# Optimization experiments

Hardware: AMD Instinct MI355X
Metric: run time of the kernel (lower is better)

The kernel has to match this reference:

```python
import jax, jax.numpy as jnp
import numpy as np

NUM_EVT = 8192
NUM_SEVT = 16384
EMBED_DIM = 128


def setup_inputs() -> dict:
    key = jax.random.key(0)
    k_adj, k_sub, k_evt, k_w = jax.random.split(key, 4)
    adj = jax.random.uniform(k_adj, (NUM_EVT, NUM_SEVT), dtype=jnp.float32)
    subevent = jax.random.normal(k_sub, (NUM_SEVT, EMBED_DIM), dtype=jnp.float32)
    event = jax.random.normal(k_evt, (NUM_EVT, EMBED_DIM), dtype=jnp.float32)
    # attn_fc: Linear(2*D -> 1, bias=False), xavier_uniform; stored flat as [2*D]
    bound = float(np.sqrt(6.0 / (2 * EMBED_DIM + 1)))
    attn_w = jax.random.uniform(k_w, (2 * EMBED_DIM,), dtype=jnp.float32,
                                minval=-bound, maxval=bound)
    return {"adj": adj, "subevent": subevent, "event": event, "attn_w": attn_w}


def reference(adj, subevent, event, attn_w):
    D = subevent.shape[-1]
    # concat order in torch forward: [sevt, evt] -> first D weights hit subevent
    a_s, a_e = attn_w[:D], attn_w[D:]
    s_proj = subevent @ a_s            # [S]
    e_proj = event @ a_e               # [E]
    # score(e,s) = LeakyReLU( attn_fc([adj*sub_s ; adj*evt_e]) )
    #            = LeakyReLU( adj[e,s] * (e_proj[e] + s_proj[s]) )
    scores = jax.nn.leaky_relu(adj * (e_proj[:, None] + s_proj[None, :]), 0.2)  # [E,S]
    attn = jax.nn.softmax(scores, axis=-1)                                      # [E,S]
    # sum_s attn[e,s] * (adj[e,s] * subevent[s])
    sevt_evt = (attn * adj) @ subevent                                          # [E,D]
    out = (event + sevt_evt) * 0.5
    return out.astype(subevent.dtype)
```

## Files before the change

### kernel.cpp

```cpp
#include <hip/hip_runtime.h>

typedef __attribute__((ext_vector_type(4))) float float4v;
typedef __attribute__((ext_vector_type(8))) short short8;

#define NEVT 8192
#define NSEVT 16384
#define DIM 128
#define BM 16
#define BK 128
#define NTILE (NSEVT / BK)

__device__ __forceinline__ unsigned f2bf(float f) {
  unsigned u = __builtin_bit_cast(unsigned, f);
  return (u + 0x7FFFu + ((u >> 16) & 1u)) >> 16;
}

__global__ void proj_kernel(const float* __restrict__ event,
                            const float* __restrict__ subevent,
                            const float* __restrict__ attn_w,
                            float* __restrict__ eproj,
                            float* __restrict__ sproj) {
  int gw = (int)((blockIdx.x * blockDim.x + threadIdx.x) >> 6);
  int lane = threadIdx.x & 63;
  const float* row;
  const float* w;
  float* outp;
  if (gw < NEVT) {
    row = event + (size_t)gw * DIM;
    w = attn_w + DIM;
    outp = eproj + gw;
  } else {
    row = subevent + (size_t)(gw - NEVT) * DIM;
    w = attn_w;
    outp = sproj + (gw - NEVT);
  }
  float2 x = *(const float2*)(row + lane * 2);
  float2 ww = *(const float2*)(w + lane * 2);
  float p = x.x * ww.x + x.y * ww.y;
#pragma unroll
  for (int off = 32; off > 0; off >>= 1) p += __shfl_down(p, off, 64);
  if (lane == 0) *outp = p;
}

__global__ void frag_kernel(const float* __restrict__ sub,
                            unsigned short* __restrict__ frag) {
  int tid = blockIdx.x * 256 + threadIdx.x;
  int lane = tid & 63;
  int db = (tid >> 6) & 7;
  int kt = tid >> 9;
  int r0 = kt * 32 + ((lane >> 4) << 3);
  int col = db * 16 + (lane & 15);
  unsigned pk[4];
#pragma unroll
  for (int jj = 0; jj < 4; ++jj) {
    unsigned lo = f2bf(sub[(size_t)(r0 + 2 * jj) * DIM + col]);
    unsigned hi = f2bf(sub[(size_t)(r0 + 2 * jj + 1) * DIM + col]);
    pk[jj] = lo | (hi << 16);
  }
  uint4 v = {pk[0], pk[1], pk[2], pk[3]};
  *(uint4*)(frag + (size_t)tid * 8) = v;
}

__global__ __launch_bounds__(256, 2) void fused_kernel(
    const float* __restrict__ adj, const float* __restrict__ event,
    const unsigned short* __restrict__ subfrag, const float* __restrict__ eproj,
    const float* __restrict__ sproj, float* __restrict__ out) {
  __shared__ unsigned short P[2][BM][132];
  __shared__ float dsum[BM][32];

  const int t = threadIdx.x;
  const int lane = t & 63;
  const int wave = t >> 6;
  const int r0 = blockIdx.x * BM;
  const int rA = t >> 5;
  const int cL = (t & 31) * 4;
  const int m = lane & 15;
  const int q = lane >> 4;

  const float ep0 = eproj[r0 + rA];
  const float ep1 = eproj[r0 + rA + 8];

  const float* adj0 = adj + (size_t)(r0 + rA) * NSEVT + cL;
  const float* adj1 = adj + (size_t)(r0 + rA + 8) * NSEVT + cL;

  float4v a0 = *(const float4v*)(adj0);
  float4v a1 = *(const float4v*)(adj1);
  float4v sp = *(const float4v*)(sproj + cL);

  float4v acc0 = {0.f, 0.f, 0.f, 0.f};
  float4v acc1 = {0.f, 0.f, 0.f, 0.f};
  float d0 = 0.f, d1 = 0.f;

  for (int tile = 0; tile < NTILE; ++tile) {
    short8 bf[4][2];
#pragma unroll
    for (int ks = 0; ks < 4; ++ks) {
#pragma unroll
      for (int i = 0; i < 2; ++i) {
        size_t off =
            ((size_t)((tile * 4 + ks) * 8 + (wave * 2 + i)) * 64 + lane) * 8;
        bf[ks][i] = *(const short8*)(subfrag + off);
      }
    }
    float4v na0 = a0, na1 = a1, nsp = sp;
    if (tile + 1 < NTILE) {
      na0 = *(const float4v*)(adj0 + (size_t)(tile + 1) * BK);
      na1 = *(const float4v*)(adj1 + (size_t)(tile + 1) * BK);
      nsp = *(const float4v*)(sproj + (tile + 1) * BK + cL);
    }
    unsigned pkA0, pkA1, pkB0, pkB1;
    {
      float w[4];
#pragma unroll
      for (int c = 0; c < 4; ++c) {
        float x = a0[c] * (ep0 + sp[c]);
        float y = fmaxf(x, 0.2f * x);
        float p = __builtin_amdgcn_exp2f(y * 1.442695040888963f);
        d0 += p;
        w[c] = p * a0[c];
      }
      pkA0 = f2bf(w[0]) | (f2bf(w[1]) << 16);
      pkA1 = f2bf(w[2]) | (f2bf(w[3]) << 16);
#pragma unroll
      for (int c = 0; c < 4; ++c) {
        float x = a1[c] * (ep1 + sp[c]);
        float y = fmaxf(x, 0.2f * x);
        float p = __builtin_amdgcn_exp2f(y * 1.442695040888963f);
        d1 += p;
        w[c] = p * a1[c];
      }
      pkB0 = f2bf(w[0]) | (f2bf(w[1]) << 16);
      pkB1 = f2bf(w[2]) | (f2bf(w[3]) << 16);
    }
    const int buf = tile & 1;
    uint2 v0 = {pkA0, pkA1};
    *(uint2*)&P[buf][rA][cL] = v0;
    uint2 v1 = {pkB0, pkB1};
    *(uint2*)&P[buf][rA + 8][cL] = v1;

    __syncthreads();

#pragma unroll
    for (int ks = 0; ks < 4; ++ks) {
      const unsigned short* ap = &P[buf][m][q * 8 + ks * 32];
      uint2 lo = *(const uint2*)(ap);
      uint2 hi = *(const uint2*)(ap + 4);
      uint4 au = {lo.x, lo.y, hi.x, hi.y};
      short8 af = __builtin_bit_cast(short8, au);
      acc0 = __builtin_amdgcn_mfma_f32_16x16x32_bf16(af, bf[ks][0], acc0, 0, 0, 0);
      acc1 = __builtin_amdgcn_mfma_f32_16x16x32_bf16(af, bf[ks][1], acc1, 0, 0, 0);
    }
    a0 = na0;
    a1 = na1;
    sp = nsp;
  }

  dsum[rA][t & 31] = d0;
  dsum[rA + 8][t & 31] = d1;
  __syncthreads();
  if (t < BM) {
    float s = 0.f;
#pragma unroll
    for (int k = 0; k < 32; ++k) s += dsum[t][k];
    dsum[t][0] = s;
  }
  __syncthreads();

  float rd[4];
#pragma unroll
  for (int r = 0; r < 4; ++r) rd[r] = 1.0f / dsum[q * 4 + r][0];

#pragma unroll
  for (int i = 0; i < 2; ++i) {
    int dim = wave * 32 + i * 16 + m;
#pragma unroll
    for (int r = 0; r < 4; ++r) {
      int row = r0 + q * 4 + r;
      float num = (i == 0) ? acc0[r] : acc1[r];
      out[(size_t)row * DIM + dim] =
          (event[(size_t)row * DIM + dim] + num * rd[r]) * 0.5f;
    }
  }
}

extern "C" void kernel_launch(void* const* d_in, const int* in_sizes, int n_in,
                              void* d_out, int out_size, void* d_ws,
                              size_t ws_size, hipStream_t stream) {
  const float* adj = (const float*)d_in[0];
  const float* subevent = (const float*)d_in[1];
  const float* event = (const float*)d_in[2];
  const float* attn_w = (const float*)d_in[3];
  float* out = (float*)d_out;

  unsigned short* subfrag = (unsigned short*)d_ws;
  float* eproj = (float*)((char*)d_ws + (size_t)NSEVT * DIM * 2);
  float* sproj = eproj + NEVT;

  proj_kernel<<<(NEVT + NSEVT) / 4, 256, 0, stream>>>(event, subevent, attn_w,
                                                      eproj, sproj);
  frag_kernel<<<(NSEVT / 32) * 8 * 64 / 256, 256, 0, stream>>>(subevent,
                                                               subfrag);
  fused_kernel<<<NEVT / BM, 256, 0, stream>>>(adj, event, subfrag, eproj,
                                              sproj, out);
}
```

Baseline: 761.0 us.

## Enlarge row tile to 64 and split the S dimension across blocks with a combine pass

The row tile grows from 16 to 64 with 512 threads per block, so each bf16 subevent fragment loaded from global memory feeds four MFMA row tiles instead of one. The S dimension is also split four ways across blocks, which keeps the grid at 512 blocks. Each block writes partial numerators and denominators to workspace, and a new combine kernel sums them, normalises, and adds the event term. The aim is to cut the redundant subfrag traffic, at the cost of an extra kernel launch and a round trip of partial results through memory.

After: 736.0 us. -3.3%, faster.

```diff
diff --git a/kernel.cpp b/kernel.cpp
--- a/kernel.cpp
+++ b/kernel.cpp
@@ -6,9 +6,11 @@
 #define NEVT 8192
 #define NSEVT 16384
 #define DIM 128
-#define BM 16
+#define BM 64
 #define BK 128
-#define NTILE (NSEVT / BK)
+#define SPLIT 4
+#define CPW (NSEVT / SPLIT)
+#define TPW (CPW / BK)
 
 __device__ __forceinline__ unsigned f2bf(float f) {
   unsigned u = __builtin_bit_cast(unsigned, f);
@@ -61,126 +63,145 @@
   *(uint4*)(frag + (size_t)tid * 8) = v;
 }
 
-__global__ __launch_bounds__(256, 2) void fused_kernel(
-    const float* __restrict__ adj, const float* __restrict__ event,
-    const unsigned short* __restrict__ subfrag, const float* __restrict__ eproj,
-    const float* __restrict__ sproj, float* __restrict__ out) {
+__global__ __launch_bounds__(512, 4) void fused_kernel(
+    const float* __restrict__ adj, const unsigned short* __restrict__ subfrag,
+    const float* __restrict__ eproj, const float* __restrict__ sproj,
+    float* __restrict__ num_ws, float* __restrict__ den_ws) {
   __shared__ unsigned short P[2][BM][132];
-  __shared__ float dsum[BM][32];
+  __shared__ float dsum[BM][8];
 
   const int t = threadIdx.x;
   const int lane = t & 63;
   const int wave = t >> 6;
-  const int r0 = blockIdx.x * BM;
-  const int rA = t >> 5;
-  const int cL = (t & 31) * 4;
+  const int mb = blockIdx.x & 127;
+  const int s = blockIdx.x >> 7;
+  const int r = t >> 3;
+  const int c8 = t & 7;
+  const int cL = c8 * 4;
+  const int row = mb * BM + r;
+  const int colbase = s * CPW;
+
+  const float ep = eproj[row];
+  const float* adjp = adj + (size_t)row * NSEVT + colbase + cL;
+  const float* spp = sproj + colbase + cL;
+
+  float4v a[4], sp[4];
+#pragma unroll
+  for (int j = 0; j < 4; ++j) {
+    a[j] = *(const float4v*)(adjp + 32 * j);
+    sp[j] = *(const float4v*)(spp + 32 * j);
+  }
+  float4v acc[4];
+#pragma unroll
+  for (int mt = 0; mt < 4; ++mt) acc[mt] = (float4v){0.f, 0.f, 0.f, 0.f};
+  float d = 0.f;
+
   const int m = lane & 15;
   const int q = lane >> 4;
 
-  const float ep0 = eproj[r0 + rA];
-  const float ep1 = eproj[r0 + rA + 8];
-
-  const float* adj0 = adj + (size_t)(r0 + rA) * NSEVT + cL;
-  const float* adj1 = adj + (size_t)(r0 + rA + 8) * NSEVT + cL;
-
-  float4v a0 = *(const float4v*)(adj0);
-  float4v a1 = *(const float4v*)(adj1);
-  float4v sp = *(const float4v*)(sproj + cL);
-
-  float4v acc0 = {0.f, 0.f, 0.f, 0.f};
-  float4v acc1 = {0.f, 0.f, 0.f, 0.f};
-  float d0 = 0.f, d1 = 0.f;
-
-  for (int tile = 0; tile < NTILE; ++tile) {
-    short8 bf[4][2];
+  for (int tile = 0; tile < TPW; ++tile) {
+    const int tg = s * TPW + tile;
+    short8 bfr[4];
 #pragma unroll
     for (int ks = 0; ks < 4; ++ks) {
-#pragma unroll
-      for (int i = 0; i < 2; ++i) {
-        size_t off =
-            ((size_t)((tile * 4 + ks) * 8 + (wave * 2 + i)) * 64 + lane) * 8;
-        bf[ks][i] = *(const short8*)(subfrag + off);
-      }
-    }
-    float4v na0 = a0, na1 = a1, nsp = sp;
-    if (tile + 1 < NTILE) {
-      na0 = *(const float4v*)(adj0 + (size_t)(tile + 1) * BK);
-      na1 = *(const float4v*)(adj1 + (size_t)(tile + 1) * BK);
-      nsp = *(const float4v*)(sproj + (tile + 1) * BK + cL);
-    }
-    unsigned pkA0, pkA1, pkB0, pkB1;
-    {
+      size_t off = ((size_t)((tg * 4 + ks) * 8 + wave) * 64 + lane) * 8;
+      bfr[ks] = *(const short8*)(subfrag + off);
+    }
+    float4v na[4], nsp[4];
+    if (tile + 1 < TPW) {
+#pragma unroll
+      for (int j = 0; j < 4; ++j) {
+        na[j] = *(const float4v*)(adjp + (size_t)(tile + 1) * BK + 32 * j);
+        nsp[j] = *(const float4v*)(spp + (tile + 1) * BK + 32 * j);
+      }
+    } else {
+#pragma unroll
+      for (int j = 0; j < 4; ++j) {
+        na[j] = a[j];
+        nsp[j] = sp[j];
+      }
+    }
+    const int buf = tile & 1;
+#pragma unroll
+    for (int j = 0; j < 4; ++j) {
       float w[4];
 #pragma unroll
       for (int c = 0; c < 4; ++c) {
-        float x = a0[c] * (ep0 + sp[c]);
+        float x = a[j][c] * (ep + sp[j][c]);
         float y = fmaxf(x, 0.2f * x);
         float p = __builtin_amdgcn_exp2f(y * 1.442695040888963f);
-        d0 += p;
-        w[c] = p * a0[c];
-      }
-      pkA0 = f2bf(w[0]) | (f2bf(w[1]) << 16);
-      pkA1 = f2bf(w[2]) | (f2bf(w[3]) << 16);
-#pragma unroll
-      for (int c = 0; c < 4; ++c) {
-        float x = a1[c] * (ep1 + sp[c]);
-        float y = fmaxf(x, 0.2f * x);
-        float p = __builtin_amdgcn_exp2f(y * 1.442695040888963f);
-        d1 += p;
-        w[c] = p * a1[c];
-      }
-      pkB0 = f2bf(w[0]) | (f2bf(w[1]) << 16);
-      pkB1 = f2bf(w[2]) | (f2bf(w[3]) << 16);
-    }
-    const int buf = tile & 1;
-    uint2 v0 = {pkA0, pkA1};
-    *(uint2*)&P[buf][rA][cL] = v0;
-    uint2 v1 = {pkB0, pkB1};
-    *(uint2*)&P[buf][rA + 8][cL] = v1;
+        d += p;
+        w[c] = p * a[j][c];
+      }
+      uint2 v = {f2bf(w[0]) | (f2bf(w[1]) << 16),
+                 f2bf(w[2]) | (f2bf(w[3]) << 16)};
+      *(uint2*)&P[buf][r][cL + 32 * j] = v;
+    }
 
     __syncthreads();
 
 #pragma unroll
     for (int ks = 0; ks < 4; ++ks) {
-      const unsigned short* ap = &P[buf][m][q * 8 + ks * 32];
-      uint2 lo = *(const uint2*)(ap);
-      uint2 hi = *(const uint2*)(ap + 4);
-      uint4 au = {lo.x, lo.y, hi.x, hi.y};
-      short8 af = __builtin_bit_cast(short8, au);
-      acc0 = __builtin_amdgcn_mfma_f32_16x16x32_bf16(af, bf[ks][0], acc0, 0, 0, 0);
-      acc1 = __builtin_amdgcn_mfma_f32_16x16x32_bf16(af, bf[ks][1], acc1, 0, 0, 0);
-    }
-    a0 = na0;
-    a1 = na1;
-    sp = nsp;
-  }
-
-  dsum[rA][t & 31] = d0;
-  dsum[rA + 8][t & 31] = d1;
+#pragma unroll
+      for (int mt = 0; mt < 4; ++mt) {
+        const unsigned short* ap = &P[buf][mt * 16 + m][ks * 32 + q * 8];
+        uint2 lo = *(const uint2*)(ap);
+        uint2 hi = *(const uint2*)(ap + 4);
+        uint4 au = {lo.x, lo.y, hi.x, hi.y};
+        short8 af = __builtin_bit_cast(short8, au);
+        acc[mt] =
+            __builtin_amdgcn_mfma_f32_16x16x32_bf16(af, bfr[ks], acc[mt], 0, 0, 0);
+      }
+    }
+#pragma unroll
+    for (int j = 0; j < 4; ++j) {
+      a[j] = na[j];
+      sp[j] = nsp[j];
+    }
+  }
+
+  dsum[r][c8] = d;
   __syncthreads();
   if (t < BM) {
-    float s = 0.f;
-#pragma unroll
-    for (int k = 0; k < 32; ++k) s += dsum[t][k];
-    dsum[t][0] = s;
-  }
-  __syncthreads();
-
-  float rd[4];
-#pragma unroll
-  for (int r = 0; r < 4; ++r) rd[r] = 1.0f / dsum[q * 4 + r][0];
-
-#pragma unroll
-  for (int i = 0; i < 2; ++i) {
-    int dim = wave * 32 + i * 16 + m;
-#pragma unroll
-    for (int r = 0; r < 4; ++r) {
-      int row = r0 + q * 4 + r;
-      float num = (i == 0) ? acc0[r] : acc1[r];
-      out[(size_t)row * DIM + dim] =
-          (event[(size_t)row * DIM + dim] + num * rd[r]) * 0.5f;
-    }
-  }
+    float ssum = 0.f;
+#pragma unroll
+    for (int k = 0; k < 8; ++k) ssum += dsum[t][k];
+    den_ws[(size_t)s * NEVT + mb * BM + t] = ssum;
+  }
+
+  float* nump = num_ws + (size_t)s * NEVT * DIM;
+#pragma unroll
+  for (int mt = 0; mt < 4; ++mt) {
+#pragma unroll
+    for (int rg = 0; rg < 4; ++rg) {
+      int rl = mt * 16 + q * 4 + rg;
+      nump[(size_t)(mb * BM + rl) * DIM + wave * 16 + m] = acc[mt][rg];
+    }
+  }
+}
+
+__global__ void combine_kernel(const float* __restrict__ event,
+                               const float* __restrict__ num_ws,
+                               const float* __restrict__ den_ws,
+                               float* __restrict__ out) {
+  int gid = blockIdx.x * 256 + threadIdx.x;
+  int base = gid * 4;
+  int row = base >> 7;
+  int col = base & 127;
+  float4v n = {0.f, 0.f, 0.f, 0.f};
+  float den = 0.f;
+#pragma unroll
+  for (int s = 0; s < SPLIT; ++s) {
+    float4v v = *(const float4v*)(num_ws + ((size_t)s * NEVT + row) * DIM + col);
+    n = n + v;
+    den += den_ws[(size_t)s * NEVT + row];
+  }
+  float4v ev = *(const float4v*)(event + (size_t)row * DIM + col);
+  float rdn = 1.0f / den;
+  float4v o;
+#pragma unroll
+  for (int c = 0; c < 4; ++c) o[c] = (ev[c] + n[c] * rdn) * 0.5f;
+  *(float4v*)(out + (size_t)row * DIM + col) = o;
 }
 
 extern "C" void kernel_launch(void* const* d_in, const int* in_sizes, int n_in,
@@ -192,14 +213,23 @@
   const float* attn_w = (const float*)d_in[3];
   float* out = (float*)d_out;
 
-  unsigned short* subfrag = (unsigned short*)d_ws;
-  float* eproj = (float*)((char*)d_ws + (size_t)NSEVT * DIM * 2);
-  float* sproj = eproj + NEVT;
+  char* w = (char*)d_ws;
+  unsigned short* subfrag = (unsigned short*)w;
+  w += (size_t)NSEVT * DIM * 2;
+  float* eproj = (float*)w;
+  w += (size_t)NEVT * 4;
+  float* sproj = (float*)w;
+  w += (size_t)NSEVT * 4;
+  float* num_ws = (float*)w;
+  w += (size_t)SPLIT * NEVT * DIM * 4;
+  float* den_ws = (float*)w;
 
   proj_kernel<<<(NEVT + NSEVT) / 4, 256, 0, stream>>>(event, subevent, attn_w,
                                                       eproj, sproj);
   frag_kernel<<<(NSEVT / 32) * 8 * 64 / 256, 256, 0, stream>>>(subevent,
                                                                subfrag);
-  fused_kernel<<<NEVT / BM, 256, 0, stream>>>(adj, event, subfrag, eproj,
-                                              sproj, out);
-}
+  fused_kernel<<<128 * SPLIT, 512, 0, stream>>>(adj, subfrag, eproj, sproj,
+                                                num_ws, den_ws);
+  combine_kernel<<<NEVT * DIM / 4 / 256, 256, 0, stream>>>(event, num_ws,
+                                                           den_ws, out);
+}
```
